# Optimization experiments

Hardware: AMD Instinct MI355X
Metric: run time of the kernel (lower is better)

## Reference

```python
import jax, jax.numpy as jnp
import numpy as np

N_HEAD = 16
NEG = -1e30  # large negative stand-in for -inf (safe under autodiff/softmax)


def setup_inputs() -> dict:
    key = jax.random.key(0)
    ks = jax.random.split(key, 6)
    B, T, C = 4, 1024, 1024
    x = jax.random.normal(ks[0], (B, T, C), jnp.float32)
    W_attn = jax.random.normal(ks[1], (C, 3 * C), jnp.float32) * 0.02
    b_attn = jnp.zeros((3 * C,), jnp.float32)
    W_proj = jax.random.normal(ks[2], (C, C), jnp.float32) * 0.02
    b_proj = jnp.zeros((C,), jnp.float32)
    sparsity_ratios = jnp.full((N_HEAD,), 0.6, jnp.float32)  # Parameter init
    gumbel_temp = jnp.ones((N_HEAD,), jnp.float32)           # Parameter init
    noise_u = jax.random.uniform(ks[3], (B, N_HEAD, T, T), jnp.float32)
    return dict(x=x, W_attn=W_attn, b_attn=b_attn, W_proj=W_proj, b_proj=b_proj,
                sparsity_ratios=sparsity_ratios, gumbel_temp=gumbel_temp, noise_u=noise_u)


def reference(x, W_attn, b_attn, W_proj, b_proj, sparsity_ratios, gumbel_temp, noise_u):
    B, T, C = x.shape
    nH = N_HEAD
    hd = C // nH

    qkv = x @ W_attn + b_attn                      # [B,T,3C]
    q, k, v = jnp.split(qkv, 3, axis=-1)
    q = q.reshape(B, T, nH, hd).transpose(0, 2, 1, 3)   # [B,nH,T,hd]
    k = k.reshape(B, T, nH, hd).transpose(0, 2, 1, 3)
    v = v.reshape(B, T, nH, hd).transpose(0, 2, 1, 3)

    att = jnp.einsum('bhqd,bhkd->bhqk', q, k) / jnp.sqrt(jnp.float32(hd))  # [B,nH,T,T]
    t_idx = jnp.arange(T)
    causal = (t_idx[:, None] >= t_idx[None, :])[None, None]  # [1,1,T,T]
    att_safe = jnp.where(causal, att, 0.0)

    # per-head sparsity knobs (detached via .item() in the original)
    ratio = jax.lax.stop_gradient(jax.nn.sigmoid(sparsity_ratios))          # (nH,)
    temp = jax.lax.stop_gradient(jax.nn.softplus(gumbel_temp) + 0.1)        # (nH,)

    # per-row top-k size: k_t = max(1, int((t+1)*ratio_h))  -> (nH,T)
    k_per = jnp.maximum(1, jnp.floor((t_idx[None, :] + 1).astype(jnp.float32) * ratio[:, None]).astype(jnp.int32))

    # gumbel-perturbed logits over valid (causal) positions
    g = -jnp.log(-jnp.log(noise_u + 1e-8) + 1e-8)
    gl = (att_safe + g) / temp[None, :, None, None]
    gl = jnp.where(causal, gl, NEG)

    # rank of each position within its row (descending); noise breaks ties a.s.
    ranks = jnp.argsort(jnp.argsort(-gl, axis=-1), axis=-1)
    selected = (ranks < k_per[None, :, :, None]) & causal

    # soft values: softmax of gumbel logits restricted to the selected set
    sv = jax.nn.softmax(jnp.where(selected, gl, NEG), axis=-1)
    sparse = jnp.where(selected, att_safe * sv, 0.0)

    # row t=0 (single valid logit): copied through unchanged
    row0 = (t_idx == 0)[None, None, :, None]
    col0 = (t_idx == 0)[None, None, None, :]
    sparse = jnp.where(row0, jnp.where(col0, att_safe, 0.0), sparse)

    # final softmax over the FULL row (zeros at unselected positions, as in torch)
    p = jax.nn.softmax(sparse, axis=-1)
    y = jnp.einsum('bhqk,bhkd->bhqd', p, v)        # [B,nH,T,hd]
    y = y.transpose(0, 2, 1, 3).reshape(B, T, C)
    return y @ W_proj + b_proj
```

## Files before the change

kernel.cpp:

```cpp
#include <hip/hip_runtime.h>
#include <math.h>

#define T_SEQ 1024
#define NH 16
#define HD 64

typedef __attribute__((ext_vector_type(8))) short bf16x8;
typedef __attribute__((ext_vector_type(4))) float f32x4;

__device__ __forceinline__ unsigned fkey(float x) {
  unsigned u = __float_as_uint(x);
  return (u & 0x80000000u) ? ~u : (u | 0x80000000u);
}

__device__ __forceinline__ float wredmax(float v) {
#pragma unroll
  for (int m = 1; m < 64; m <<= 1) v = fmaxf(v, __shfl_xor(v, m));
  return v;
}
__device__ __forceinline__ float wredsum(float v) {
#pragma unroll
  for (int m = 1; m < 64; m <<= 1) v += __shfl_xor(v, m);
  return v;
}

__device__ __forceinline__ unsigned short f2bf(float f) {
  unsigned u = __float_as_uint(f);
  return (unsigned short)((u + 0x7fffu + ((u >> 16) & 1u)) >> 16);
}
__device__ __forceinline__ float bf2f(unsigned short h) {
  return __uint_as_float(((unsigned)h) << 16);
}

__device__ __forceinline__ void gl_lds16(const void* g, void* l) {
  __builtin_amdgcn_global_load_lds(
      (const __attribute__((address_space(1))) unsigned int*)g,
      (__attribute__((address_space(3))) unsigned int*)l,
      16, 0, 0);
}

__global__ __launch_bounds__(256) void k_split_a2(const float* __restrict__ X,
                                                  unsigned short* __restrict__ A2) {
  const int idx = blockIdx.x * 256 + threadIdx.x;
  const int m = idx >> 8;
  const int c4 = idx & 255;
  const float4 x = ((const float4*)(X + ((size_t)m << 10)))[c4];
  const float xs[4] = {x.x, x.y, x.z, x.w};
  unsigned short hh[4], ll[4];
#pragma unroll
  for (int j = 0; j < 4; ++j) {
    hh[j] = f2bf(xs[j]);
    ll[j] = f2bf(xs[j] - bf2f(hh[j]));
  }
  ushort4* dst = (ushort4*)(A2 + ((size_t)m << 11));
  dst[c4] = make_ushort4(hh[0], hh[1], hh[2], hh[3]);
  dst[c4 + 256] = make_ushort4(ll[0], ll[1], ll[2], ll[3]);
}

__global__ __launch_bounds__(256) void k_split_b2(const float* __restrict__ W,
                                                  unsigned short* __restrict__ Bh,
                                                  unsigned short* __restrict__ Bl,
                                                  int N, int K) {
  __shared__ unsigned short shi[32][33];
  __shared__ unsigned short slo[32][33];
  const int n0 = blockIdx.x * 32, k0 = blockIdx.y * 32;
  const int ty = threadIdx.x >> 3;
  const int tx = threadIdx.x & 7;
  const float4 w4 = *(const float4*)(W + (size_t)(k0 + ty) * N + n0 + (tx << 2));
  const float wv[4] = {w4.x, w4.y, w4.z, w4.w};
#pragma unroll
  for (int j = 0; j < 4; ++j) {
    const unsigned short hs = f2bf(wv[j]);
    shi[ty][(tx << 2) + j] = hs;
    slo[ty][(tx << 2) + j] = f2bf(wv[j] - bf2f(hs));
  }
  __syncthreads();
  const int n = n0 + ty;
  const ushort4 h = make_ushort4(shi[(tx << 2) + 0][ty], shi[(tx << 2) + 1][ty],
                                 shi[(tx << 2) + 2][ty], shi[(tx << 2) + 3][ty]);
  const ushort4 l = make_ushort4(slo[(tx << 2) + 0][ty], slo[(tx << 2) + 1][ty],
                                 slo[(tx << 2) + 2][ty], slo[(tx << 2) + 3][ty]);
  ((ushort4*)(Bh + (size_t)n * K))[(k0 >> 2) + tx] = h;
  ((ushort4*)(Bl + (size_t)n * K))[(k0 >> 2) + tx] = l;
}

__global__ __launch_bounds__(256) void k_qkv3(
    const unsigned short* __restrict__ A, const unsigned short* __restrict__ Bh,
    const unsigned short* __restrict__ Bl, const float* __restrict__ bias,
    unsigned short* __restrict__ Q2, unsigned short* __restrict__ Kht,
    unsigned short* __restrict__ Klt, unsigned short* __restrict__ Vht,
    unsigned short* __restrict__ Vlt) {
  __shared__ unsigned short Ahs[128 * 32], Als[128 * 32], Bhs[128 * 32], Bls[128 * 32];
  const int tid = threadIdx.x, lane = tid & 63, w = tid >> 6;
  const int m0 = blockIdx.y * 128, n0 = blockIdx.x * 128;
  const int wr = (w >> 1) << 6, wc = (w & 1) << 6;
  f32x4 acc[4][4];
#pragma unroll
  for (int i = 0; i < 4; ++i)
#pragma unroll
    for (int j = 0; j < 4; ++j) acc[i][j] = (f32x4){0.f, 0.f, 0.f, 0.f};

  const int lrow = lane >> 2, lk = (lane & 3) << 3;
  const int r0 = (w << 5) + lrow, r1 = r0 + 16;
  const unsigned short* gah0 = A + (size_t)(m0 + r0) * 2048 + lk;
  const unsigned short* gah1 = A + (size_t)(m0 + r1) * 2048 + lk;
  const unsigned short* gbh0 = Bh + (size_t)(n0 + r0) * 1024 + lk;
  const unsigned short* gbh1 = Bh + (size_t)(n0 + r1) * 1024 + lk;
  const unsigned short* gbl0 = Bl + (size_t)(n0 + r0) * 1024 + lk;
  const unsigned short* gbl1 = Bl + (size_t)(n0 + r1) * 1024 + lk;
  unsigned short* lah0 = Ahs + (w << 10) + (lane << 3);
  unsigned short* lal0 = Als + (w << 10) + (lane << 3);
  unsigned short* lbh0 = Bhs + (w << 10) + (lane << 3);
  unsigned short* lbl0 = Bls + (w << 10) + (lane << 3);
  const int fcol = lane & 15, koff = (lane >> 4) << 3;

  for (int k0 = 0; k0 < 1024; k0 += 32) {
    __syncthreads();
    gl_lds16(gah0 + k0, lah0);        gl_lds16(gah1 + k0, lah0 + 512);
    gl_lds16(gah0 + 1024 + k0, lal0); gl_lds16(gah1 + 1024 + k0, lal0 + 512);
    gl_lds16(gbh0 + k0, lbh0);        gl_lds16(gbh1 + k0, lbh0 + 512);
    gl_lds16(gbl0 + k0, lbl0);        gl_lds16(gbl1 + k0, lbl0 + 512);
    __syncthreads();
    bf16x8 afh[4], afl[4], bfh[4], bfl[4];
#pragma unroll
    for (int i = 0; i < 4; ++i) {
      const int off = ((wr + (i << 4) + fcol) << 5) + koff;
      afh[i] = *(const bf16x8*)&Ahs[off];
      afl[i] = *(const bf16x8*)&Als[off];
    }
#pragma unroll
    for (int j = 0; j < 4; ++j) {
      const int off = ((wc + (j << 4) + fcol) << 5) + koff;
      bfh[j] = *(const bf16x8*)&Bhs[off];
      bfl[j] = *(const bf16x8*)&Bls[off];
    }
#pragma unroll
    for (int i = 0; i < 4; ++i)
#pragma unroll
      for (int j = 0; j < 4; ++j) {
        acc[i][j] = __builtin_amdgcn_mfma_f32_16x16x32_bf16(afh[i], bfh[j], acc[i][j], 0, 0, 0);
        acc[i][j] = __builtin_amdgcn_mfma_f32_16x16x32_bf16(afh[i], bfl[j], acc[i][j], 0, 0, 0);
        acc[i][j] = __builtin_amdgcn_mfma_f32_16x16x32_bf16(afl[i], bfh[j], acc[i][j], 0, 0, 0);
      }
  }

  const int qd = lane >> 4;
#pragma unroll
  for (int j = 0; j < 4; ++j) {
    const int n = n0 + wc + (j << 4) + fcol;
    const float bv = bias[n];
    const int which = n >> 10;
    const int c = n & 1023;
    const int hsel = c >> 6, cc = c & 63;
#pragma unroll
    for (int i = 0; i < 4; ++i) {
#pragma unroll
      for (int r = 0; r < 4; ++r) {
        const int m = m0 + wr + (i << 4) + (qd << 2) + r;
        const int b = m >> 10, t = m & 1023;
        const int z = b * NH + hsel;
        const float v = acc[i][j][r] + bv;
        const unsigned short hi = f2bf(v);
        const unsigned short lo = f2bf(v - bf2f(hi));
        if (which == 0) {
          unsigned short* q = Q2 + (((size_t)z * T_SEQ + t) << 7) + cc;
          q[0] = hi; q[64] = lo;
        } else if (which == 1) {
          const size_t o = (((size_t)z * T_SEQ + t) << 6) + cc;
          Kht[o] = hi; Klt[o] = lo;
        } else {
          const size_t o = (((size_t)z * HD + cc) << 10) + t;
          Vht[o] = hi; Vlt[o] = lo;
        }
      }
    }
  }
}

__global__ __launch_bounds__(256) void k_att3(
    const unsigned short* __restrict__ Q2, const unsigned short* __restrict__ Kht,
    const unsigned short* __restrict__ Klt, float* __restrict__ ATT) {
  __shared__ unsigned short Ahs[128 * 32], Als[128 * 32], Bhs[128 * 32], Bls[128 * 32];
  const int tid = threadIdx.x, lane = tid & 63, w = tid >> 6;
  const int z = blockIdx.z;
  const unsigned short* A = Q2 + ((size_t)z * T_SEQ << 7);
  const unsigned short* Bh = Kht + ((size_t)z * T_SEQ << 6);
  const unsigned short* Bl = Klt + ((size_t)z * T_SEQ << 6);
  float* Az = ATT + (size_t)z * T_SEQ * T_SEQ;
  const int m0 = blockIdx.y * 128, n0 = blockIdx.x * 128;
  const int wr = (w >> 1) << 6, wc = (w & 1) << 6;
  f32x4 acc[4][4];
#pragma unroll
  for (int i = 0; i < 4; ++i)
#pragma unroll
    for (int j = 0; j < 4; ++j) acc[i][j] = (f32x4){0.f, 0.f, 0.f, 0.f};

  const int lrow = lane >> 2, lk = (lane & 3) << 3;
  const int r0 = (w << 5) + lrow, r1 = r0 + 16;
  const unsigned short* gah0 = A + ((size_t)(m0 + r0) << 7) + lk;
  const unsigned short* gah1 = A + ((size_t)(m0 + r1) << 7) + lk;
  const unsigned short* gbh0 = Bh + ((size_t)(n0 + r0) << 6) + lk;
  const unsigned short* gbh1 = Bh + ((size_t)(n0 + r1) << 6) + lk;
  const unsigned short* gbl0 = Bl + ((size_t)(n0 + r0) << 6) + lk;
  const unsigned short* gbl1 = Bl + ((size_t)(n0 + r1) << 6) + lk;
  unsigned short* lah0 = Ahs + (w << 10) + (lane << 3);
  unsigned short* lal0 = Als + (w << 10) + (lane << 3);
  unsigned short* lbh0 = Bhs + (w << 10) + (lane << 3);
  unsigned short* lbl0 = Bls + (w << 10) + (lane << 3);
  const int fcol = lane & 15, koff = (lane >> 4) << 3;

#pragma unroll
  for (int k0 = 0; k0 < 64; k0 += 32) {
    __syncthreads();
    gl_lds16(gah0 + k0, lah0);      gl_lds16(gah1 + k0, lah0 + 512);
    gl_lds16(gah0 + 64 + k0, lal0); gl_lds16(gah1 + 64 + k0, lal0 + 512);
    gl_lds16(gbh0 + k0, lbh0);      gl_lds16(gbh1 + k0, lbh0 + 512);
    gl_lds16(gbl0 + k0, lbl0);      gl_lds16(gbl1 + k0, lbl0 + 512);
    __syncthreads();
    bf16x8 afh[4], afl[4], bfh[4], bfl[4];
#pragma unroll
    for (int i = 0; i < 4; ++i) {
      const int off = ((wr + (i << 4) + fcol) << 5) + koff;
      afh[i] = *(const bf16x8*)&Ahs[off];
      afl[i] = *(const bf16x8*)&Als[off];
    }
#pragma unroll
    for (int j = 0; j < 4; ++j) {
      const int off = ((wc + (j << 4) + fcol) << 5) + koff;
      bfh[j] = *(const bf16x8*)&Bhs[off];
      bfl[j] = *(const bf16x8*)&Bls[off];
    }
#pragma unroll
    for (int i = 0; i < 4; ++i)
#pragma unroll
      for (int j = 0; j < 4; ++j) {
        acc[i][j] = __builtin_amdgcn_mfma_f32_16x16x32_bf16(afh[i], bfh[j], acc[i][j], 0, 0, 0);
        acc[i][j] = __builtin_amdgcn_mfma_f32_16x16x32_bf16(afh[i], bfl[j], acc[i][j], 0, 0, 0);
        acc[i][j] = __builtin_amdgcn_mfma_f32_16x16x32_bf16(afl[i], bfh[j], acc[i][j], 0, 0, 0);
      }
  }

  const int qd = lane >> 4;
#pragma unroll
  for (int i = 0; i < 4; ++i)
#pragma unroll
    for (int r = 0; r < 4; ++r) {
      const int m = wr + (i << 4) + (qd << 2) + r;
#pragma unroll
      for (int j = 0; j < 4; ++j)
        Az[(size_t)(m0 + m) * T_SEQ + (n0 + wc + (j << 4) + fcol)] = acc[i][j][r] * 0.125f;
    }
}

template<int NSEG>
__device__ __forceinline__ void select_body(
    const float4* __restrict__ arow, const float4* __restrict__ urow,
    ushort4* __restrict__ prow, const int t, const int lane,
    const unsigned k, const float invtemp) {
  constexpr int NE = 4 * NSEG;

  float av[NE], gv[NE];
  unsigned key[NE];
#pragma unroll
  for (int s = 0; s < NSEG; ++s) {
    const float4 a4 = arow[(s << 6) + lane];
    const float4 u4 = urow[(s << 6) + lane];
    const float aa[4] = {a4.x, a4.y, a4.z, a4.w};
    const float uu[4] = {u4.x, u4.y, u4.z, u4.w};
#pragma unroll
    for (int j = 0; j < 4; ++j) {
      const int e = (s << 2) + j;
      const int col = (s << 8) + (lane << 2) + j;
      const float g = -__logf(-__logf(uu[j] + 1e-8f) + 1e-8f);
      av[e] = aa[j];
      gv[e] = (col <= t) ? (aa[j] + g) * invtemp : -INFINITY;
      key[e] = fkey(gv[e]);
    }
  }

  unsigned th = 0u;
#pragma unroll
  for (int b = 31; b >= 0; --b) {
    const unsigned cand = th | (1u << b);
    unsigned c = 0;
#pragma unroll
    for (int e = 0; e < NE; ++e)
      c += (unsigned)__popcll(__ballot(key[e] >= cand));
    if (c >= k) th = cand;
  }
  const unsigned tau = th;

  unsigned cnt_gt = 0;
#pragma unroll
  for (int e = 0; e < NE; ++e)
    cnt_gt += (unsigned)__popcll(__ballot(key[e] > tau));
  const unsigned need = k - cnt_gt;

  const unsigned long long below = ((unsigned long long)1 << lane) - 1ull;
  unsigned rank[NE];
  unsigned base = 0;
#pragma unroll
  for (int s = 0; s < NSEG; ++s) {
    unsigned lanecnt = 0, tot = 0, own = 0;
    unsigned long long B[4];
#pragma unroll
    for (int j = 0; j < 4; ++j) {
      B[j] = __ballot(key[(s << 2) + j] == tau);
      lanecnt += (unsigned)__popcll(B[j] & below);
      tot += (unsigned)__popcll(B[j]);
    }
#pragma unroll
    for (int j = 0; j < 4; ++j) {
      rank[(s << 2) + j] = base + lanecnt + own;
      own += (key[(s << 2) + j] == tau) ? 1u : 0u;
    }
    base += tot;
  }

  bool sel[NE];
#pragma unroll
  for (int e = 0; e < NE; ++e)
    sel[e] = (key[e] > tau) | ((key[e] == tau) & (rank[e] < need));

  float lm = -INFINITY;
#pragma unroll
  for (int e = 0; e < NE; ++e) lm = fmaxf(lm, gv[e]);
  const float m = wredmax(lm);

  float ex[NE];
  float ps = 0.f;
#pragma unroll
  for (int e = 0; e < NE; ++e) {
    ex[e] = sel[e] ? __expf(gv[e] - m) : 0.f;
    ps += ex[e];
  }
  const float S = wredsum(ps);
  const float invS = 1.f / S;

  float sp[NE];
#pragma unroll
  for (int e = 0; e < NE; ++e) sp[e] = sel[e] ? av[e] * ex[e] * invS : 0.f;

  float lM = 0.f;
#pragma unroll
  for (int e = 0; e < NE; ++e) lM = fmaxf(lM, sp[e]);
  const float M = wredmax(lM);

  float pe[NE];
  float lz = 0.f;
#pragma unroll
  for (int e = 0; e < NE; ++e) { pe[e] = __expf(sp[e] - M); lz += pe[e]; }
  const float ez = __expf(0.f - M);
  const float Z = wredsum(lz) + (float)(1024 - 256 * NSEG) * ez;
  const float invZ = 1.f / Z;

#pragma unroll
  for (int s = 0; s < NSEG; ++s) {
    unsigned short hh[4], ll[4];
#pragma unroll
    for (int j = 0; j < 4; ++j) {
      const float p = pe[(s << 2) + j] * invZ;
      hh[j] = f2bf(p);
      ll[j] = f2bf(p - bf2f(hh[j]));
    }
    prow[(s << 6) + lane] = make_ushort4(hh[0], hh[1], hh[2], hh[3]);
    prow[256 + (s << 6) + lane] = make_ushort4(ll[0], ll[1], ll[2], ll[3]);
  }
  if (NSEG < 4) {
    const float pz = ez * invZ;
    const unsigned short hz = f2bf(pz);
    const unsigned short lz2 = f2bf(pz - bf2f(hz));
    const ushort4 hv = make_ushort4(hz, hz, hz, hz);
    const ushort4 lv = make_ushort4(lz2, lz2, lz2, lz2);
#pragma unroll
    for (int s = NSEG; s < 4; ++s) {
      prow[(s << 6) + lane] = hv;
      prow[256 + (s << 6) + lane] = lv;
    }
  }
}

__global__ __launch_bounds__(256, 4) void k_select(
    const float* __restrict__ ATT, unsigned short* __restrict__ P2,
    const float* __restrict__ NOISE,
    const float* __restrict__ SR, const float* __restrict__ GT) {
  const int tid = threadIdx.x;
  const int lane = tid & 63;
  const int row = (blockIdx.x << 2) | (tid >> 6);
  const int t = row & 1023;
  const int h = (row >> 10) & 15;

  const float ratio = 1.f / (1.f + __expf(-SR[h]));
  const float temp = log1pf(__expf(GT[h])) + 0.1f;
  const float invtemp = 1.f / temp;
  const int kf = (int)floorf((float)(t + 1) * ratio);
  const unsigned k = (unsigned)(kf < 1 ? 1 : kf);

  const float4* arow = (const float4*)(ATT + ((size_t)row << 10));
  const float4* urow = (const float4*)(NOISE + ((size_t)row << 10));
  ushort4* prow = (ushort4*)(P2 + ((size_t)row << 11));

  switch (t >> 8) {
    case 0:  select_body<1>(arow, urow, prow, t, lane, k, invtemp); break;
    case 1:  select_body<2>(arow, urow, prow, t, lane, k, invtemp); break;
    case 2:  select_body<3>(arow, urow, prow, t, lane, k, invtemp); break;
    default: select_body<4>(arow, urow, prow, t, lane, k, invtemp); break;
  }
}

__global__ __launch_bounds__(256) void k_pv3(
    const unsigned short* __restrict__ P2, const unsigned short* __restrict__ Vht,
    const unsigned short* __restrict__ Vlt, unsigned short* __restrict__ Y2) {
  __shared__ unsigned short Ahs[128 * 32], Als[128 * 32], Bhs[64 * 32], Bls[64 * 32];
  const int tid = threadIdx.x, lane = tid & 63, w = tid >> 6;
  const int z = blockIdx.z;
  const int b = z >> 4, h = z & 15;
  const unsigned short* A = P2 + ((size_t)z * T_SEQ << 11);
  const unsigned short* Bh = Vht + ((size_t)z * HD << 10);
  const unsigned short* Bl = Vlt + ((size_t)z * HD << 10);
  const int m0 = blockIdx.x * 128;
  const int wr = (w >> 1) << 6, wc = (w & 1) << 5;
  f32x4 acc[4][2];
#pragma unroll
  for (int i = 0; i < 4; ++i)
#pragma unroll
    for (int j = 0; j < 2; ++j) acc[i][j] = (f32x4){0.f, 0.f, 0.f, 0.f};

  const int lrow = lane >> 2, lk = (lane & 3) << 3;
  const int ra0 = (w << 5) + lrow, ra1 = ra0 + 16;
  const int rb = (w << 4) + lrow;
  const unsigned short* gah0 = A + ((size_t)(m0 + ra0) << 11) + lk;
  const unsigned short* gah1 = A + ((size_t)(m0 + ra1) << 11) + lk;
  const unsigned short* gbh = Bh + ((size_t)rb << 10) + lk;
  const unsigned short* gbl = Bl + ((size_t)rb << 10) + lk;
  unsigned short* lah0 = Ahs + (w << 10) + (lane << 3);
  unsigned short* lal0 = Als + (w << 10) + (lane << 3);
  unsigned short* lbh = Bhs + (w << 9) + (lane << 3);
  unsigned short* lbl = Bls + (w << 9) + (lane << 3);
  const int fcol = lane & 15, koff = (lane >> 4) << 3;

  for (int k0 = 0; k0 < 1024; k0 += 32) {
    __syncthreads();
    gl_lds16(gah0 + k0, lah0);        gl_lds16(gah1 + k0, lah0 + 512);
    gl_lds16(gah0 + 1024 + k0, lal0); gl_lds16(gah1 + 1024 + k0, lal0 + 512);
    gl_lds16(gbh + k0, lbh);
    gl_lds16(gbl + k0, lbl);
    __syncthreads();
    bf16x8 afh[4], afl[4], bfh[2], bfl[2];
#pragma unroll
    for (int i = 0; i < 4; ++i) {
      const int off = ((wr + (i << 4) + fcol) << 5) + koff;
      afh[i] = *(const bf16x8*)&Ahs[off];
      afl[i] = *(const bf16x8*)&Als[off];
    }
#pragma unroll
    for (int j = 0; j < 2; ++j) {
      const int off = ((wc + (j << 4) + fcol) << 5) + koff;
      bfh[j] = *(const bf16x8*)&Bhs[off];
      bfl[j] = *(const bf16x8*)&Bls[off];
    }
#pragma unroll
    for (int i = 0; i < 4; ++i)
#pragma unroll
      for (int j = 0; j < 2; ++j) {
        acc[i][j] = __builtin_amdgcn_mfma_f32_16x16x32_bf16(afh[i], bfh[j], acc[i][j], 0, 0, 0);
        acc[i][j] = __builtin_amdgcn_mfma_f32_16x16x32_bf16(afh[i], bfl[j], acc[i][j], 0, 0, 0);
        acc[i][j] = __builtin_amdgcn_mfma_f32_16x16x32_bf16(afl[i], bfh[j], acc[i][j], 0, 0, 0);
      }
  }

  const int qd = lane >> 4;
#pragma unroll
  for (int j = 0; j < 2; ++j) {
    const int d = wc + (j << 4) + fcol;
    const int c = (h << 6) + d;
#pragma unroll
    for (int i = 0; i < 4; ++i) {
#pragma unroll
      for (int r = 0; r < 4; ++r) {
        const int tq = m0 + wr + (i << 4) + (qd << 2) + r;
        const float v = acc[i][j][r];
        const unsigned short hi = f2bf(v);
        const unsigned short lo = f2bf(v - bf2f(hi));
        unsigned short* y = Y2 + (((size_t)(b * T_SEQ + tq)) << 11) + c;
        y[0] = hi; y[1024] = lo;
      }
    }
  }
}

__global__ __launch_bounds__(256) void k_proj3(
    const unsigned short* __restrict__ A, const unsigned short* __restrict__ Bh,
    const unsigned short* __restrict__ Bl, const float* __restrict__ bias,
    float* __restrict__ OUT) {
  __shared__ unsigned short Ahs[128 * 32], Als[128 * 32], Bhs[128 * 32], Bls[128 * 32];
  const int tid = threadIdx.x, lane = tid & 63, w = tid >> 6;
  const int m0 = blockIdx.y * 128, n0 = blockIdx.x * 128;
  const int wr = (w >> 1) << 6, wc = (w & 1) << 6;
  f32x4 acc[4][4];
#pragma unroll
  for (int i = 0; i < 4; ++i)
#pragma unroll
    for (int j = 0; j < 4; ++j) acc[i][j] = (f32x4){0.f, 0.f, 0.f, 0.f};

  const int lrow = lane >> 2, lk = (lane & 3) << 3;
  const int r0 = (w << 5) + lrow, r1 = r0 + 16;
  const unsigned short* gah0 = A + ((size_t)(m0 + r0) << 11) + lk;
  const unsigned short* gah1 = A + ((size_t)(m0 + r1) << 11) + lk;
  const unsigned short* gbh0 = Bh + ((size_t)(n0 + r0) << 10) + lk;
  const unsigned short* gbh1 = Bh + ((size_t)(n0 + r1) << 10) + lk;
  const unsigned short* gbl0 = Bl + ((size_t)(n0 + r0) << 10) + lk;
  const unsigned short* gbl1 = Bl + ((size_t)(n0 + r1) << 10) + lk;
  unsigned short* lah0 = Ahs + (w << 10) + (lane << 3);
  unsigned short* lal0 = Als + (w << 10) + (lane << 3);
  unsigned short* lbh0 = Bhs + (w << 10) + (lane << 3);
  unsigned short* lbl0 = Bls + (w << 10) + (lane << 3);
  const int fcol = lane & 15, koff = (lane >> 4) << 3;

  for (int k0 = 0; k0 < 1024; k0 += 32) {
    __syncthreads();
    gl_lds16(gah0 + k0, lah0);        gl_lds16(gah1 + k0, lah0 + 512);
    gl_lds16(gah0 + 1024 + k0, lal0); gl_lds16(gah1 + 1024 + k0, lal0 + 512);
    gl_lds16(gbh0 + k0, lbh0);        gl_lds16(gbh1 + k0, lbh0 + 512);
    gl_lds16(gbl0 + k0, lbl0);        gl_lds16(gbl1 + k0, lbl0 + 512);
    __syncthreads();
    bf16x8 afh[4], afl[4], bfh[4], bfl[4];
#pragma unroll
    for (int i = 0; i < 4; ++i) {
      const int off = ((wr + (i << 4) + fcol) << 5) + koff;
      afh[i] = *(const bf16x8*)&Ahs[off];
      afl[i] = *(const bf16x8*)&Als[off];
    }
#pragma unroll
    for (int j = 0; j < 4; ++j) {
      const int off = ((wc + (j << 4) + fcol) << 5) + koff;
      bfh[j] = *(const bf16x8*)&Bhs[off];
      bfl[j] = *(const bf16x8*)&Bls[off];
    }
#pragma unroll
    for (int i = 0; i < 4; ++i)
#pragma unroll
      for (int j = 0; j < 4; ++j) {
        acc[i][j] = __builtin_amdgcn_mfma_f32_16x16x32_bf16(afh[i], bfh[j], acc[i][j], 0, 0, 0);
        acc[i][j] = __builtin_amdgcn_mfma_f32_16x16x32_bf16(afh[i], bfl[j], acc[i][j], 0, 0, 0);
        acc[i][j] = __builtin_amdgcn_mfma_f32_16x16x32_bf16(afl[i], bfh[j], acc[i][j], 0, 0, 0);
      }
  }

  const int qd = lane >> 4;
#pragma unroll
  for (int j = 0; j < 4; ++j) {
    const int n = n0 + wc + (j << 4) + fcol;
    const float bv = bias[n];
#pragma unroll
    for (int i = 0; i < 4; ++i)
#pragma unroll
      for (int r = 0; r < 4; ++r) {
        const int m = m0 + wr + (i << 4) + (qd << 2) + r;
        OUT[((size_t)m << 10) + n] = acc[i][j][r] + bv;
      }
  }
}

extern "C" void kernel_launch(void* const* d_in, const int* in_sizes, int n_in,
                              void* d_out, int out_size, void* d_ws, size_t ws_size,
                              hipStream_t stream) {
  const float* x      = (const float*)d_in[0];
  const float* W_attn = (const float*)d_in[1];
  const float* b_attn = (const float*)d_in[2];
  const float* W_proj = (const float*)d_in[3];
  const float* b_proj = (const float*)d_in[4];
  const float* sr     = (const float*)d_in[5];
  const float* gt     = (const float*)d_in[6];
  const float* noise  = (const float*)d_in[7];

  char* base = (char*)d_ws;
  float*          ATT = (float*)base;
  unsigned short* A2q = (unsigned short*)base;
  unsigned short* Bhq = (unsigned short*)(base + 16777216);
  unsigned short* Blq = (unsigned short*)(base + 23068672);
  unsigned short* P2  = (unsigned short*)base;
  unsigned short* Q2  = (unsigned short*)(base + 268435456);
  unsigned short* Wph = (unsigned short*)(base + 268435456);
  unsigned short* Wpl = (unsigned short*)(base + 270532608);
  unsigned short* Kht = (unsigned short*)(base + 285212672);
  unsigned short* Klt = (unsigned short*)(base + 293601280);
  unsigned short* Y2  = (unsigned short*)(base + 285212672);
  unsigned short* Vht = (unsigned short*)(base + 301989888);
  unsigned short* Vlt = (unsigned short*)(base + 310378496);
  float* OUT = (float*)d_out;

  k_split_a2<<<dim3(4096),     256, 0, stream>>>(x, A2q);
  k_split_b2<<<dim3(96, 32),   256, 0, stream>>>(W_attn, Bhq, Blq, 3072, 1024);
  k_qkv3    <<<dim3(24, 32),   256, 0, stream>>>(A2q, Bhq, Blq, b_attn, Q2, Kht, Klt, Vht, Vlt);
  k_att3    <<<dim3(8, 8, 64), 256, 0, stream>>>(Q2, Kht, Klt, ATT);
  k_split_b2<<<dim3(32, 32),   256, 0, stream>>>(W_proj, Wph, Wpl, 1024, 1024);
  k_select  <<<dim3(16384),    256, 0, stream>>>(ATT, P2, noise, sr, gt);
  k_pv3     <<<dim3(8, 1, 64), 256, 0, stream>>>(P2, Vht, Vlt, Y2);
  k_proj3   <<<dim3(8, 32),    256, 0, stream>>>(Y2, Wph, Wpl, b_proj, OUT);
}
```

Baseline: 798.6 us.

## Skip causal-masked tiles in QK and PV using constant-tail suffix sums

QK^T now launches only the lower-triangular 128x128 tiles, decoding a linear block index into row and column tiles. In the select kernel, the constant softmax tail for fully masked 256-column segments is stored as one scalar per row instead of being written into P. PV then iterates only over the live K range and adds that scalar times a precomputed suffix sum of V, which k_vsuf computes per head. This removes roughly half of the QK and PV MFMA work plus the P tail writes, at the cost of one extra small kernel and some epilogue arithmetic.

```diff
diff --git a/kernel.cpp b/kernel.cpp
--- a/kernel.cpp
+++ b/kernel.cpp
@@ -177,17 +177,49 @@
   }
 }
 
+__global__ __launch_bounds__(256) void k_vsuf(const unsigned short* __restrict__ Vht,
+                                              const unsigned short* __restrict__ Vlt,
+                                              float* __restrict__ SUF) {
+  const int z = blockIdx.x;
+  const int tid = threadIdx.x, lane = tid & 63, w = tid >> 6;
+  const unsigned short* vh = Vht + ((size_t)z * HD << 10);
+  const unsigned short* vl = Vlt + ((size_t)z * HD << 10);
+  for (int d = w; d < 64; d += 4) {
+    const unsigned short* rh = vh + ((size_t)d << 10);
+    const unsigned short* rl = vl + ((size_t)d << 10);
+    float segs[3];
+#pragma unroll
+    for (int sgi = 0; sgi < 3; ++sgi) {
+      const int kb = 256 + (sgi << 8) + (lane << 2);
+      const ushort4 h4 = *(const ushort4*)(rh + kb);
+      const ushort4 l4 = *(const ushort4*)(rl + kb);
+      float acc = bf2f(h4.x) + bf2f(h4.y) + bf2f(h4.z) + bf2f(h4.w)
+                + bf2f(l4.x) + bf2f(l4.y) + bf2f(l4.z) + bf2f(l4.w);
+      segs[sgi] = wredsum(acc);
+    }
+    if (lane == 0) {
+      float* o = SUF + (size_t)z * 3 * 64;
+      o[0 * 64 + d] = segs[0] + segs[1] + segs[2];
+      o[1 * 64 + d] = segs[1] + segs[2];
+      o[2 * 64 + d] = segs[2];
+    }
+  }
+}
+
 __global__ __launch_bounds__(256) void k_att3(
     const unsigned short* __restrict__ Q2, const unsigned short* __restrict__ Kht,
     const unsigned short* __restrict__ Klt, float* __restrict__ ATT) {
   __shared__ unsigned short Ahs[128 * 32], Als[128 * 32], Bhs[128 * 32], Bls[128 * 32];
   const int tid = threadIdx.x, lane = tid & 63, w = tid >> 6;
-  const int z = blockIdx.z;
+  const int z = blockIdx.y;
+  int ti = blockIdx.x, mt = 0;
+  while (ti >= mt + 1) { ti -= mt + 1; ++mt; }
+  const int m0 = mt << 7, n0 = ti << 7;
+
   const unsigned short* A = Q2 + ((size_t)z * T_SEQ << 7);
   const unsigned short* Bh = Kht + ((size_t)z * T_SEQ << 6);
   const unsigned short* Bl = Klt + ((size_t)z * T_SEQ << 6);
   float* Az = ATT + (size_t)z * T_SEQ * T_SEQ;
-  const int m0 = blockIdx.y * 128, n0 = blockIdx.x * 128;
   const int wr = (w >> 1) << 6, wc = (w & 1) << 6;
   f32x4 acc[4][4];
 #pragma unroll
@@ -255,8 +287,8 @@
 template<int NSEG>
 __device__ __forceinline__ void select_body(
     const float4* __restrict__ arow, const float4* __restrict__ urow,
-    ushort4* __restrict__ prow, const int t, const int lane,
-    const unsigned k, const float invtemp) {
+    ushort4* __restrict__ prow, float* __restrict__ CT, const int row,
+    const int t, const int lane, const unsigned k, const float invtemp) {
   constexpr int NE = 4 * NSEG;
 
   float av[NE], gv[NE];
@@ -367,22 +399,13 @@
     prow[256 + (s << 6) + lane] = make_ushort4(ll[0], ll[1], ll[2], ll[3]);
   }
   if (NSEG < 4) {
-    const float pz = ez * invZ;
-    const unsigned short hz = f2bf(pz);
-    const unsigned short lz2 = f2bf(pz - bf2f(hz));
-    const ushort4 hv = make_ushort4(hz, hz, hz, hz);
-    const ushort4 lv = make_ushort4(lz2, lz2, lz2, lz2);
-#pragma unroll
-    for (int s = NSEG; s < 4; ++s) {
-      prow[(s << 6) + lane] = hv;
-      prow[256 + (s << 6) + lane] = lv;
-    }
+    if (lane == 0) CT[row] = ez * invZ;
   }
 }
 
 __global__ __launch_bounds__(256, 4) void k_select(
     const float* __restrict__ ATT, unsigned short* __restrict__ P2,
-    const float* __restrict__ NOISE,
+    const float* __restrict__ NOISE, float* __restrict__ CT,
     const float* __restrict__ SR, const float* __restrict__ GT) {
   const int tid = threadIdx.x;
   const int lane = tid & 63;
@@ -401,16 +424,17 @@
   ushort4* prow = (ushort4*)(P2 + ((size_t)row << 11));
 
   switch (t >> 8) {
-    case 0:  select_body<1>(arow, urow, prow, t, lane, k, invtemp); break;
-    case 1:  select_body<2>(arow, urow, prow, t, lane, k, invtemp); break;
-    case 2:  select_body<3>(arow, urow, prow, t, lane, k, invtemp); break;
-    default: select_body<4>(arow, urow, prow, t, lane, k, invtemp); break;
+    case 0:  select_body<1>(arow, urow, prow, CT, row, t, lane, k, invtemp); break;
+    case 1:  select_body<2>(arow, urow, prow, CT, row, t, lane, k, invtemp); break;
+    case 2:  select_body<3>(arow, urow, prow, CT, row, t, lane, k, invtemp); break;
+    default: select_body<4>(arow, urow, prow, CT, row, t, lane, k, invtemp); break;
   }
 }
 
 __global__ __launch_bounds__(256) void k_pv3(
     const unsigned short* __restrict__ P2, const unsigned short* __restrict__ Vht,
-    const unsigned short* __restrict__ Vlt, unsigned short* __restrict__ Y2) {
+    const unsigned short* __restrict__ Vlt, const float* __restrict__ CT,
+    const float* __restrict__ SUF, unsigned short* __restrict__ Y2) {
   __shared__ unsigned short Ahs[128 * 32], Als[128 * 32], Bhs[64 * 32], Bls[64 * 32];
   const int tid = threadIdx.x, lane = tid & 63, w = tid >> 6;
   const int z = blockIdx.z;
@@ -419,6 +443,8 @@
   const unsigned short* Bh = Vht + ((size_t)z * HD << 10);
   const unsigned short* Bl = Vlt + ((size_t)z * HD << 10);
   const int m0 = blockIdx.x * 128;
+  const int NSEG = (int)(blockIdx.x >> 1) + 1;
+  const int KLEN = NSEG << 8;
   const int wr = (w >> 1) << 6, wc = (w & 1) << 5;
   f32x4 acc[4][2];
 #pragma unroll
@@ -439,7 +465,7 @@
   unsigned short* lbl = Bls + (w << 9) + (lane << 3);
   const int fcol = lane & 15, koff = (lane >> 4) << 3;
 
-  for (int k0 = 0; k0 < 1024; k0 += 32) {
+  for (int k0 = 0; k0 < KLEN; k0 += 32) {
     __syncthreads();
     gl_lds16(gah0 + k0, lah0);        gl_lds16(gah1 + k0, lah0 + 512);
     gl_lds16(gah0 + 1024 + k0, lal0); gl_lds16(gah1 + 1024 + k0, lal0 + 512);
@@ -470,16 +496,28 @@
   }
 
   const int qd = lane >> 4;
+  float ct[4][4];
+  if (NSEG < 4) {
+    const float* ctp = CT + ((size_t)z << 10) + m0;
+#pragma unroll
+    for (int i = 0; i < 4; ++i)
+#pragma unroll
+      for (int r = 0; r < 4; ++r)
+        ct[i][r] = ctp[wr + (i << 4) + (qd << 2) + r];
+  }
 #pragma unroll
   for (int j = 0; j < 2; ++j) {
     const int d = wc + (j << 4) + fcol;
     const int c = (h << 6) + d;
+    float sv = 0.f;
+    if (NSEG < 4) sv = SUF[((size_t)z * 3 + (NSEG - 1)) * 64 + d];
 #pragma unroll
     for (int i = 0; i < 4; ++i) {
 #pragma unroll
       for (int r = 0; r < 4; ++r) {
         const int tq = m0 + wr + (i << 4) + (qd << 2) + r;
-        const float v = acc[i][j][r];
+        float v = acc[i][j][r];
+        if (NSEG < 4) v += ct[i][r] * sv;
         const unsigned short hi = f2bf(v);
         const unsigned short lo = f2bf(v - bf2f(hi));
         unsigned short* y = Y2 + (((size_t)(b * T_SEQ + tq)) << 11) + c;
@@ -588,14 +626,17 @@
   unsigned short* Y2  = (unsigned short*)(base + 285212672);
   unsigned short* Vht = (unsigned short*)(base + 301989888);
   unsigned short* Vlt = (unsigned short*)(base + 310378496);
+  float* CT  = (float*)(base + 318767104);
+  float* SUF = (float*)(base + 319029248);
   float* OUT = (float*)d_out;
 
   k_split_a2<<<dim3(4096),     256, 0, stream>>>(x, A2q);
   k_split_b2<<<dim3(96, 32),   256, 0, stream>>>(W_attn, Bhq, Blq, 3072, 1024);
   k_qkv3    <<<dim3(24, 32),   256, 0, stream>>>(A2q, Bhq, Blq, b_attn, Q2, Kht, Klt, Vht, Vlt);
-  k_att3    <<<dim3(8, 8, 64), 256, 0, stream>>>(Q2, Kht, Klt, ATT);
+  k_vsuf    <<<dim3(64),       256, 0, stream>>>(Vht, Vlt, SUF);
+  k_att3    <<<dim3(36, 64),   256, 0, stream>>>(Q2, Kht, Klt, ATT);
   k_split_b2<<<dim3(32, 32),   256, 0, stream>>>(W_proj, Wph, Wpl, 1024, 1024);
-  k_select  <<<dim3(16384),    256, 0, stream>>>(ATT, P2, noise, sr, gt);
-  k_pv3     <<<dim3(8, 1, 64), 256, 0, stream>>>(P2, Vht, Vlt, Y2);
+  k_select  <<<dim3(16384),    256, 0, stream>>>(ATT, P2, noise, CT, sr, gt);
+  k_pv3     <<<dim3(8, 1, 64), 256, 0, stream>>>(P2, Vht, Vlt, CT, SUF, Y2);
   k_proj3   <<<dim3(8, 32),    256, 0, stream>>>(Y2, Wph, Wpl, b_proj, OUT);
 }
```

Measured after the change: 815.7 us. +2.1%, slower.
